# Performance work log

Hardware: AMD Instinct MI355X
Metric: run time of the kernel (lower is better)

The kernel has to match this reference:

```python
import jax, jax.numpy as jnp
import numpy as np
from jax import lax

RATE = 2
KSIZE = 3
FUSE_K = 3
SOFTMAX_SCALE = 10.0
EPS = 1e-8


def extract_patches(x, k, s):
    """ZeroPad2d(1) then unfold: x [B,C,H,W] -> patches [B, oh*ow, C, k, k]."""
    xp = jnp.pad(x, ((0, 0), (0, 0), (1, 1), (1, 1)))
    B, C, Hp, Wp = xp.shape
    oh = (Hp - k) // s + 1
    ow = (Wp - k) // s + 1
    ii = (jnp.arange(oh) * s)[:, None] + jnp.arange(k)[None, :]   # [oh,k]
    jj = (jnp.arange(ow) * s)[:, None] + jnp.arange(k)[None, :]   # [ow,k]
    p = xp[:, :, ii[:, :, None, None], jj[None, None, :, :]]      # [B,C,oh,k,ow,k]
    p = p.transpose(0, 2, 4, 1, 3, 5).reshape(B, oh * ow, C, k, k)
    return p


def _fuse_conv(a, eye):
    # a: [B,1,N,M]; 3x3 identity-diagonal smoothing conv, padding 1
    return lax.conv_general_dilated(a, eye, (1, 1), [(1, 1), (1, 1)],
                                    dimension_numbers=('NCHW', 'OIHW', 'NCHW'))


def contextual_attention(in_data, mask):
    B, C, H, W = in_data.shape
    Cf = C // 2
    f_full = in_data[:, :Cf]          # narrow(1,0,C//2)
    b_full = in_data[:, :Cf]          # source narrows the SAME slice for b
    mask_f = mask.astype(in_data.dtype)
    rate = RATE
    kernel = 2 * rate

    # raw 4x4 patches of full-res background (deconv filters), [B,L,Cf,4,4]
    raw_w = extract_patches(b_full, kernel, rate)

    # nearest downsample by 1/rate == strided slicing
    f = f_full[:, :, ::rate, ::rate]
    b = b_full[:, :, ::rate, ::rate]
    h, w = f.shape[2], f.shape[3]
    L = h * w

    # 3x3 matching patches of downsampled background, L2-normalized per patch
    wpat = extract_patches(b, KSIZE, 1)                              # [B,L,Cf,3,3]
    norm = jnp.sqrt(jnp.sum(wpat * wpat, axis=(2, 3, 4), keepdims=True))
    wn = wpat / jnp.maximum(norm, EPS)

    # per-sample conv2d(xi, wi_normed, padding=1) == patch/patch correlation
    fp = extract_patches(f, KSIZE, 1)                                # [B,hw,Cf,3,3]
    yi = jnp.einsum('bpckl,bqckl->bqp', fp, wn).reshape(B, L, h, w)  # [B,L,h,w]

    # fuse: two diagonal 3x3 smoothing passes over the [L, h*w] score matrix
    eye = jnp.eye(FUSE_K, dtype=in_data.dtype).reshape(1, 1, FUSE_K, FUSE_K)
    A = yi.reshape(B, 1, L, h * w)
    A = _fuse_conv(A, eye)
    A = A.reshape(B, h, w, h, w).transpose(0, 2, 1, 4, 3).reshape(B, 1, w * h, w * h)
    A = _fuse_conv(A, eye)
    A = A.reshape(B, w, h, w, h).transpose(0, 2, 1, 4, 3)
    yi = A.reshape(B, L, h, w)

    # mask gate: mm = 1 where the 3x3 mask patch is all-zero
    mpat = extract_patches(mask_f, KSIZE, 1)[0]                      # [L,1,3,3]
    m_mean = jnp.mean(mpat, axis=(1, 2, 3))                          # [L]
    mm = (m_mean == 0.0).astype(in_data.dtype)[None, :, None, None]
    yi = yi * mm
    yi = jax.nn.softmax(yi * SOFTMAX_SCALE, axis=1)
    yi = yi * mm

    # conv_transpose2d(yi, raw_wi, stride=rate, padding=1) / 4 per sample
    def agg(y1, rw):
        rhs = jnp.flip(rw, (-2, -1)).transpose(1, 0, 2, 3)           # [Cf,L,4,4]
        return lax.conv_general_dilated(y1[None], rhs, (1, 1), [(2, 2), (2, 2)],
                                        lhs_dilation=(rate, rate),
                                        dimension_numbers=('NCHW', 'OIHW', 'NCHW'))[0]
    y = jax.vmap(agg)(yi, raw_w) / 4.0                               # [B,Cf,H,W]

    # masked_fill_(inv_mask, 0) == multiply by {0,1} mask, upsampled to H x W
    mask_up = jnp.repeat(jnp.repeat(mask_f, rate, axis=2), rate, axis=3)
    y = y * mask_up

    return jnp.concatenate([b_full, f_full, y], axis=1)             # [B,3*Cf,H,W]


def setup_inputs() -> dict:
    key = jax.random.key(0)
    k1, k2 = jax.random.split(key)
    in_data = jax.random.normal(k1, (2, 128, 128, 128), dtype=jnp.float32)
    mask = jax.random.randint(k2, (1, 1, 64, 64), 0, 2, dtype=jnp.int32)
    return {"in_data": in_data, "mask": mask}


def reference(in_data, mask):
    return contextual_attention(in_data, mask)
```

## Files before the change

### kernel.cpp

```cpp
#include <hip/hip_runtime.h>
#include <math.h>

#define MAX_SLOTS 64
#define L 4096

#define OFF_CNT   0
#define OFF_LIST  64
#define OFF_FSUB  512
#define OFF_K5    2230784
#define OFF_SF    4065792

__global__ __launch_bounds__(256) void k_init(const float* __restrict__ in,
                                              const int* __restrict__ mask,
                                              int* __restrict__ cnt,
                                              int* __restrict__ list,
                                              float* __restrict__ fsub,
                                              float* __restrict__ sf) {
    int idx = blockIdx.x * 256 + threadIdx.x;
    int j = idx & 63;
    int i = (idx >> 6) & 63;
    int c = (idx >> 12) & 63;
    int b = idx >> 18;
    float v = in[(((b * 128 + c) * 128) + 2 * i) * 128 + 2 * j];
    fsub[(size_t)b * 278784 + c * 4356 + (i + 1) * 66 + (j + 1)] = v;
    sf[idx] = 0.f;
    if (idx < 33280) {
        int plane = idx / 260;
        int r = idx - plane * 260;
        int pb = plane >> 6, pc = plane & 63;
        int row, col;
        if (r < 66) { row = 0; col = r; }
        else if (r < 132) { row = 65; col = r - 66; }
        else { int rr = r - 132; row = (rr >> 1) + 1; col = (rr & 1) ? 65 : 0; }
        fsub[(size_t)pb * 278784 + pc * 4356 + row * 66 + col] = 0.f;
    }
    if (blockIdx.x == 0) {
        __shared__ int lcnt;
        if (threadIdx.x == 0) lcnt = 0;
        __syncthreads();
        for (int q = threadIdx.x; q < L; q += 256) {
            int qi = q >> 6, qj = q & 63;
            bool allz = true;
            for (int dy = -1; dy <= 1; ++dy)
                for (int dx = -1; dx <= 1; ++dx) {
                    int y = qi + dy, x = qj + dx;
                    if (y >= 0 && y < 64 && x >= 0 && x < 64)
                        allz = allz && (mask[y * 64 + x] == 0);
                }
            if (allz) {
                int p = atomicAdd(&lcnt, 1);
                if (p < MAX_SLOTS) list[p] = q;
            }
        }
        __syncthreads();
        if (threadIdx.x == 0) *cnt = (lcnt < MAX_SLOTS) ? lcnt : MAX_SLOTS;
    }
}

__global__ __launch_bounds__(256) void k_mid(const int* __restrict__ cnt,
                                             const int* __restrict__ list,
                                             const float* __restrict__ fsub,
                                             float* __restrict__ K5,
                                             float* __restrict__ sf) {
    __shared__ float smem[5184];
    __shared__ int iflags[16];
    int tid = threadIdx.x;
    int blk = blockIdx.x;
    int nact = min(*cnt, MAX_SLOTS);

    if (blk < 128) {
        int slot = blk & 63, b = blk >> 6;
        if (slot >= nact) {
            for (int t = tid; t < 1600; t += 256) {
                int c = t / 25, e = t - c * 25;
                K5[(((size_t)b * 64 + c) * 64 + slot) * 28 + e] = 0.f;
            }
            return;
        }
        float* patch9 = smem;
        if (tid < 9) iflags[tid] = 0;
        __syncthreads();
        int Q = list[slot];
        const float* F = fsub + (size_t)b * 278784;
        int w = tid >> 6, lane = tid & 63;
        for (int combo = w; combo < 9; combo += 4) {
            int d2 = combo / 3 - 1, d1 = combo % 3 - 1;
            int XQ = ((Q & 63) << 6) + (Q >> 6) + d2;
            if (XQ < 0 || XQ >= L) continue;
            int YQ = ((XQ & 63) << 6) + (XQ >> 6);
            int R = YQ + d1;
            if (R < 0 || R >= L) continue;
            if (lane == 0) iflags[combo] = 1;
            int ri = R >> 6, rj = R & 63;
            const float* Fp = F + ri * 66 + rj;
            float vals[9]; float ss = 0.f;
            #pragma unroll
            for (int k = 0; k < 9; ++k) {
                int t = lane + (k << 6);
                int c = t / 9; int tap = t - c * 9;
                int dy = tap / 3, dx = tap - dy * 3;
                float v = Fp[c * 4356 + dy * 66 + dx];
                vals[k] = v; ss += v * v;
            }
            for (int o = 32; o > 0; o >>= 1) ss += __shfl_xor(ss, o);
            float inv = 1.f / fmaxf(sqrtf(ss), 1e-8f);
            float* dst = patch9 + combo * 576;
            #pragma unroll
            for (int k = 0; k < 9; ++k) dst[lane + (k << 6)] = vals[k] * inv;
        }
        __syncthreads();
        for (int t = tid; t < 1600; t += 256) {
            int c = t / 25, e = t - c * 25;
            int oy = e / 5 - 2, ox = e - (e / 5) * 5 - 2;
            float s = 0.f;
            for (int dy = -1; dy <= 1; ++dy) {
                int dd2 = oy - dy; if (dd2 < -1 || dd2 > 1) continue;
                for (int dx = -1; dx <= 1; ++dx) {
                    int dd1 = ox - dx; if (dd1 < -1 || dd1 > 1) continue;
                    int combo = (dd2 + 1) * 3 + (dd1 + 1);
                    if (iflags[combo])
                        s += patch9[combo * 576 + c * 9 + (dy + 1) * 3 + (dx + 1)];
                }
            }
            K5[(((size_t)b * 64 + c) * 64 + slot) * 28 + e] = s;
        }
        return;
    }

    int bt = blk - 128;
    int combo = bt % 9; int rest = bt / 9;
    int slot = rest & 63, b = rest >> 6;
    if (slot >= nact) return;
    int d2 = combo / 3 - 1, d1 = combo % 3 - 1;
    int Q = list[slot];
    int XQ = ((Q & 63) << 6) + (Q >> 6) + d2;
    if (XQ < 0 || XQ >= L) return;
    int YQ = ((XQ & 63) << 6) + (XQ >> 6);
    int R = YQ + d1;
    if (R < 0 || R >= L) return;
    int ri = R >> 6, rj = R & 63;
    const float* F = fsub + (size_t)b * 278784;
    float* patch = smem;
    float* red = smem + 576;
    const float* Fp = F + ri * 66 + rj;
    auto ld = [&](int t) -> float {
        int c = t / 9; int tap = t - c * 9;
        int dy = tap / 3, dx = tap - dy * 3;
        return Fp[c * 4356 + dy * 66 + dx];
    };
    float v0 = ld(tid), v1 = ld(tid + 256), v2 = (tid < 64) ? ld(tid + 512) : 0.f;
    red[tid] = v0 * v0 + v1 * v1 + v2 * v2;
    __syncthreads();
    if (tid < 64) {
        float a = red[tid] + red[tid + 64] + red[tid + 128] + red[tid + 192];
        for (int o = 32; o > 0; o >>= 1) a += __shfl_xor(a, o);
        if (tid == 0) smem[832] = 1.f / fmaxf(sqrtf(a), 1e-8f);
    }
    __syncthreads();
    float inv = smem[832];
    patch[tid] = v0 * inv; patch[tid + 256] = v1 * inv;
    if (tid < 64) patch[tid + 512] = v2 * inv;
    __syncthreads();
    if (tid >= 252) return;
    int i, j;
    if (tid < 64)       { i = 0;  j = tid; }
    else if (tid < 128) { i = 63; j = tid - 64; }
    else if (tid < 190) { i = tid - 127; j = 0; }
    else                { i = tid - 189; j = 63; }
    int P = (i << 6) + j;
    int XP = (j << 6) + i + d2;
    if (XP < 0 || XP >= L) return;
    int YP = ((XP & 63) << 6) + (XP >> 6);
    int Z = YP + d1;
    if (Z < 0 || Z >= L) return;
    int pi = Z >> 6, pj = Z & 63;
    const float* Fz = F + pi * 66 + pj;
    float dot = 0.f;
    #pragma unroll 4
    for (int c = 0; c < 64; ++c) {
        const float* Fc = Fz + c * 4356;
        const float* pc = patch + c * 9;
        dot += Fc[0] * pc[0]   + Fc[1] * pc[1]   + Fc[2] * pc[2];
        dot += Fc[66] * pc[3]  + Fc[67] * pc[4]  + Fc[68] * pc[5];
        dot += Fc[132] * pc[6] + Fc[133] * pc[7] + Fc[134] * pc[8];
    }
    atomicAdd(&sf[((size_t)b * 64 + slot) * 4096 + P], dot);
}

__global__ __launch_bounds__(256) void k_conv(const float* __restrict__ fsub,
                                              const int* __restrict__ cnt,
                                              const float* __restrict__ K5,
                                              float* __restrict__ sf) {
    int nact = min(*cnt, MAX_SLOTS);
    if (nact == 0) return;
    int wid = __builtin_amdgcn_readfirstlane(blockIdx.x * 4 + (threadIdx.x >> 6));
    int j = threadIdx.x & 63;
    int r   = 1 + (wid % 62);
    int cg2 = (wid / 62) & 15;
    int b   = wid / 992;
    int jc = min(max(j, 1), 62);
    const float* F = fsub + (size_t)b * 278784;
    int base = (r - 1) * 66 + (jc - 1);
    bool active = (j >= 1 && j <= 62);
    int P = (r << 6) + j;
    for (int s0 = 0; s0 < nact; s0 += 16) {
        float acc[16];
        #pragma unroll
        for (int s = 0; s < 16; ++s) acc[s] = 0.f;
        #pragma unroll
        for (int cc = 0; cc < 4; ++cc) {
            int c = cg2 * 4 + cc;
            const float* Fc = F + c * 4356 + base;
            float win[25];
            #pragma unroll
            for (int dy = 0; dy < 5; ++dy)
                #pragma unroll
                for (int dx = 0; dx < 5; ++dx)
                    win[dy * 5 + dx] = Fc[dy * 66 + dx];
            const float* kc = K5 + (((size_t)b * 64 + c) * 64 + s0) * 28;
            #pragma unroll
            for (int s = 0; s < 16; ++s) {
                #pragma unroll
                for (int k = 0; k < 25; ++k)
                    acc[s] += kc[s * 28 + k] * win[k];
            }
        }
        if (active) {
            int smax = min(16, nact - s0);
            for (int s = 0; s < smax; ++s)
                atomicAdd(&sf[((size_t)b * 64 + (s0 + s)) * 4096 + P], acc[s]);
        }
    }
}

__global__ __launch_bounds__(256) void k_tail(const float* __restrict__ in,
                                              const int* __restrict__ mask,
                                              const int* __restrict__ cnt,
                                              const int* __restrict__ list,
                                              const float* __restrict__ sf,
                                              float* __restrict__ out) {
    __shared__ float sw[MAX_SLOTS * 192];
    __shared__ float pat8[MAX_SLOTS * 128];
    int tid = threadIdx.x;
    int nact = min(*cnt, MAX_SLOTS);
    int up = blockIdx.x, cg8 = blockIdx.y, b = blockIdx.z;
    int c0 = cg8 * 8;
    const float* inb0 = in + (size_t)b * 2097152 + (size_t)c0 * 16384;
    const float* sfb = sf + (size_t)b * 64 * 4096;
    for (int t = tid; t < nact * 192; t += 256) {
        int s = t / 192; int rr = t - s * 192;
        int i = up - 1 + (rr >> 6); int jj = rr & 63;
        sw[t] = (i >= 0 && i < 64) ? sfb[(size_t)s * 4096 + (i << 6) + jj] : 0.f;
    }
    for (int t = tid; t < nact * 128; t += 256) {
        int s = t >> 7; int rr = t & 127;
        int cc = rr >> 4; int e = rr & 15; int aa = e >> 2; int bb = e & 3;
        int q = list[s]; int qi = q >> 6, qj = q & 63;
        int row = 2 * qi - 1 + aa, col = 2 * qj - 1 + bb;
        float v = (row >= 0 && row < 128 && col >= 0 && col < 128)
                  ? inb0[(size_t)cc * 16384 + row * 128 + col] : 0.f;
        pat8[t] = v;
    }
    __syncthreads();
    if (tid < 192 && nact > 0) {
        int i = up - 1 + (tid >> 6);
        if (i >= 0 && i < 64) {
            float M = 0.f;
            for (int s = 0; s < nact; ++s)
                M = fmaxf(M, 10.f * sw[s * 192 + tid]);
            float den = (float)(L - nact) * expf(-M);
            for (int s = 0; s < nact; ++s) {
                float e = expf(10.f * sw[s * 192 + tid] - M);
                sw[s * 192 + tid] = e;
                den += e;
            }
            float inv = 1.f / den;
            for (int s = 0; s < nact; ++s)
                sw[s * 192 + tid] *= inv;
        } else {
            for (int s = 0; s < nact; ++s) sw[s * 192 + tid] = 0.f;
        }
    }
    __syncthreads();
    int uu = tid >> 7, v = tid & 127;
    int u = up * 2 + uu;
    float y[8];
    #pragma unroll
    for (int cc = 0; cc < 8; ++cc) y[cc] = 0.f;
    if (mask[(u >> 1) * 64 + (v >> 1)] != 0 && nact > 0) {
        int pa = (u + 1) & 1, pb = (v + 1) & 1;
        int i0 = (u + 1 - pa) >> 1, j0 = (v + 1 - pb) >> 1;
        int Wp[4]; int tap[4]; bool val[4];
        #pragma unroll
        for (int di = 0; di < 2; ++di)
            #pragma unroll
            for (int dj = 0; dj < 2; ++dj) {
                int p = di * 2 + dj;
                int i = i0 - di, j = j0 - dj;
                int ii = i - (up - 1);
                val[p] = (j >= 0 && j < 64);
                Wp[p] = val[p] ? (ii * 64 + j) : 0;
                tap[p] = (pa + 2 * di) * 4 + (pb + 2 * dj);
            }
        for (int s = 0; s < nact; ++s) {
            const float* wrow = sw + s * 192;
            const float* ps = pat8 + s * 128;
            #pragma unroll
            for (int p = 0; p < 4; ++p) {
                if (!val[p]) continue;
                float wv = wrow[Wp[p]];
                #pragma unroll
                for (int cc = 0; cc < 8; ++cc)
                    y[cc] += wv * ps[cc * 16 + tap[p]];
            }
        }
        #pragma unroll
        for (int cc = 0; cc < 8; ++cc) y[cc] *= 0.25f;
    }
    size_t ob = (size_t)(b * 192) * 16384 + (size_t)u * 128 + v;
    #pragma unroll
    for (int cc = 0; cc < 8; ++cc) {
        int c = c0 + cc;
        float pval = in[(size_t)(b * 128 + c) * 16384 + u * 128 + v];
        out[ob + (size_t)c * 16384] = pval;
        out[ob + (size_t)(c + 64) * 16384] = pval;
        out[ob + (size_t)(c + 128) * 16384] = y[cc];
    }
}

extern "C" void kernel_launch(void* const* d_in, const int* in_sizes, int n_in,
                              void* d_out, int out_size, void* d_ws, size_t ws_size,
                              hipStream_t stream) {
    const float* in = (const float*)d_in[0];
    const int* mask = (const int*)d_in[1];
    float* out = (float*)d_out;
    char* ws = (char*)d_ws;
    int* cnt    = (int*)(ws + OFF_CNT);
    int* list   = (int*)(ws + OFF_LIST);
    float* fsub = (float*)(ws + OFF_FSUB);
    float* K5   = (float*)(ws + OFF_K5);
    float* sf   = (float*)(ws + OFF_SF);

    k_init<<<2048, 256, 0, stream>>>(in, mask, cnt, list, fsub, sf);
    k_mid<<<1280, 256, 0, stream>>>(cnt, list, fsub, K5, sf);
    k_conv<<<496, 256, 0, stream>>>(fsub, cnt, K5, sf);
    k_tail<<<dim3(64, 8, 2), 256, 0, stream>>>(in, mask, cnt, list, sf, out);
}
```

Before: 149.1 us.

## Chunk tail kernel over slots with per-thread online softmax to shrink LDS

The tail kernel no longer stages all active slots' score rows and patches in shared memory. It processes slots in chunks of 16, computing an online (running max/denominator) softmax per thread in a first pass and recomputing exponentials in a second pass for the aggregation. Patch data is also relaid out channel-innermost so each tap reads 8 contiguous floats. This cuts LDS from about 80KB to about 20KB to allow more resident blocks, at the cost of reloading score chunks twice and doing redundant expf per thread and tap.

```diff
diff --git a/kernel.cpp b/kernel.cpp
--- a/kernel.cpp
+++ b/kernel.cpp
@@ -233,90 +233,112 @@
     }
 }
 
+#define SCH 16
 __global__ __launch_bounds__(256) void k_tail(const float* __restrict__ in,
                                               const int* __restrict__ mask,
                                               const int* __restrict__ cnt,
                                               const int* __restrict__ list,
                                               const float* __restrict__ sf,
                                               float* __restrict__ out) {
-    __shared__ float sw[MAX_SLOTS * 192];
-    __shared__ float pat8[MAX_SLOTS * 128];
+    __shared__ float swc[SCH * 192];
+    __shared__ float patc[SCH * 128];
     int tid = threadIdx.x;
     int nact = min(*cnt, MAX_SLOTS);
     int up = blockIdx.x, cg8 = blockIdx.y, b = blockIdx.z;
     int c0 = cg8 * 8;
     const float* inb0 = in + (size_t)b * 2097152 + (size_t)c0 * 16384;
     const float* sfb = sf + (size_t)b * 64 * 4096;
-    for (int t = tid; t < nact * 192; t += 256) {
-        int s = t / 192; int rr = t - s * 192;
-        int i = up - 1 + (rr >> 6); int jj = rr & 63;
-        sw[t] = (i >= 0 && i < 64) ? sfb[(size_t)s * 4096 + (i << 6) + jj] : 0.f;
-    }
-    for (int t = tid; t < nact * 128; t += 256) {
-        int s = t >> 7; int rr = t & 127;
-        int cc = rr >> 4; int e = rr & 15; int aa = e >> 2; int bb = e & 3;
-        int q = list[s]; int qi = q >> 6, qj = q & 63;
-        int row = 2 * qi - 1 + aa, col = 2 * qj - 1 + bb;
-        float v = (row >= 0 && row < 128 && col >= 0 && col < 128)
-                  ? inb0[(size_t)cc * 16384 + row * 128 + col] : 0.f;
-        pat8[t] = v;
-    }
-    __syncthreads();
-    if (tid < 192 && nact > 0) {
-        int i = up - 1 + (tid >> 6);
-        if (i >= 0 && i < 64) {
-            float M = 0.f;
-            for (int s = 0; s < nact; ++s)
-                M = fmaxf(M, 10.f * sw[s * 192 + tid]);
-            float den = (float)(L - nact) * expf(-M);
-            for (int s = 0; s < nact; ++s) {
-                float e = expf(10.f * sw[s * 192 + tid] - M);
-                sw[s * 192 + tid] = e;
-                den += e;
-            }
-            float inv = 1.f / den;
-            for (int s = 0; s < nact; ++s)
-                sw[s * 192 + tid] *= inv;
-        } else {
-            for (int s = 0; s < nact; ++s) sw[s * 192 + tid] = 0.f;
-        }
-    }
-    __syncthreads();
+
     int uu = tid >> 7, v = tid & 127;
     int u = up * 2 + uu;
-    float y[8];
-    #pragma unroll
-    for (int cc = 0; cc < 8; ++cc) y[cc] = 0.f;
-    if (mask[(u >> 1) * 64 + (v >> 1)] != 0 && nact > 0) {
+    bool hole = (mask[(u >> 1) * 64 + (v >> 1)] != 0) && (nact > 0);
+    int Wp[4]; int tap[4]; bool val[4];
+    {
         int pa = (u + 1) & 1, pb = (v + 1) & 1;
         int i0 = (u + 1 - pa) >> 1, j0 = (v + 1 - pb) >> 1;
-        int Wp[4]; int tap[4]; bool val[4];
         #pragma unroll
         for (int di = 0; di < 2; ++di)
             #pragma unroll
             for (int dj = 0; dj < 2; ++dj) {
                 int p = di * 2 + dj;
                 int i = i0 - di, j = j0 - dj;
+                val[p] = (i >= 0 && i < 64 && j >= 0 && j < 64);
                 int ii = i - (up - 1);
-                val[p] = (j >= 0 && j < 64);
                 Wp[p] = val[p] ? (ii * 64 + j) : 0;
                 tap[p] = (pa + 2 * di) * 4 + (pb + 2 * dj);
             }
-        for (int s = 0; s < nact; ++s) {
-            const float* wrow = sw + s * 192;
-            const float* ps = pat8 + s * 128;
-            #pragma unroll
-            for (int p = 0; p < 4; ++p) {
-                if (!val[p]) continue;
-                float wv = wrow[Wp[p]];
+    }
+
+    float M[4] = {0.f, 0.f, 0.f, 0.f};
+    float den[4];
+    #pragma unroll
+    for (int p = 0; p < 4; ++p) den[p] = (float)(L - nact);
+    for (int sc0 = 0; sc0 < nact; sc0 += SCH) {
+        int csz = min(SCH, nact - sc0);
+        __syncthreads();
+        for (int t = tid; t < csz * 192; t += 256) {
+            int s = t / 192; int rr = t - s * 192;
+            int i = up - 1 + (rr >> 6); int jj = rr & 63;
+            swc[t] = (i >= 0 && i < 64) ? sfb[(size_t)(sc0 + s) * 4096 + (i << 6) + jj] : 0.f;
+        }
+        __syncthreads();
+        if (hole) {
+            for (int s = 0; s < csz; ++s) {
+                const float* wrow = swc + s * 192;
                 #pragma unroll
-                for (int cc = 0; cc < 8; ++cc)
-                    y[cc] += wv * ps[cc * 16 + tap[p]];
-            }
-        }
-        #pragma unroll
-        for (int cc = 0; cc < 8; ++cc) y[cc] *= 0.25f;
-    }
+                for (int p = 0; p < 4; ++p) {
+                    if (!val[p]) continue;
+                    float l = 10.f * wrow[Wp[p]];
+                    if (l > M[p]) { den[p] *= expf(M[p] - l); M[p] = l; }
+                    den[p] += expf(l - M[p]);
+                }
+            }
+        }
+    }
+    float inv[4];
+    #pragma unroll
+    for (int p = 0; p < 4; ++p) inv[p] = val[p] ? 1.f / den[p] : 0.f;
+
+    float y[8];
+    #pragma unroll
+    for (int cc = 0; cc < 8; ++cc) y[cc] = 0.f;
+    for (int sc0 = 0; sc0 < nact; sc0 += SCH) {
+        int csz = min(SCH, nact - sc0);
+        __syncthreads();
+        for (int t = tid; t < csz * 192; t += 256) {
+            int s = t / 192; int rr = t - s * 192;
+            int i = up - 1 + (rr >> 6); int jj = rr & 63;
+            swc[t] = (i >= 0 && i < 64) ? sfb[(size_t)(sc0 + s) * 4096 + (i << 6) + jj] : 0.f;
+        }
+        for (int t = tid; t < csz * 128; t += 256) {
+            int s = t >> 7; int rr = t & 127;
+            int tp = rr >> 3; int cc = rr & 7; int aa = tp >> 2; int bb = tp & 3;
+            int q = list[sc0 + s]; int qi = q >> 6, qj = q & 63;
+            int row = 2 * qi - 1 + aa, col = 2 * qj - 1 + bb;
+            float pv = (row >= 0 && row < 128 && col >= 0 && col < 128)
+                       ? inb0[(size_t)cc * 16384 + row * 128 + col] : 0.f;
+            patc[t] = pv;
+        }
+        __syncthreads();
+        if (hole) {
+            for (int s = 0; s < csz; ++s) {
+                const float* wrow = swc + s * 192;
+                const float* ps = patc + s * 128;
+                #pragma unroll
+                for (int p = 0; p < 4; ++p) {
+                    if (!val[p]) continue;
+                    float wv = expf(10.f * wrow[Wp[p]] - M[p]) * inv[p];
+                    const float* pp = ps + tap[p] * 8;
+                    #pragma unroll
+                    for (int cc = 0; cc < 8; ++cc)
+                        y[cc] += wv * pp[cc];
+                }
+            }
+        }
+    }
+    #pragma unroll
+    for (int cc = 0; cc < 8; ++cc) y[cc] *= 0.25f;
+
     size_t ob = (size_t)(b * 192) * 16384 + (size_t)u * 128 + v;
     #pragma unroll
     for (int cc = 0; cc < 8; ++cc) {
```

After: 153.5 us. 3.0% more time.
